# Performance work log

Hardware: AMD Instinct MI355X
Metric: run time of the kernel (lower is better)

Reference implementation:

```python
import jax, jax.numpy as jnp
import numpy as np

B, S, D, H, MEM, P = 32, 512, 768, 8, 768, 3
DK = D // H
LN_EPS = 1e-6


def _layer_norm(x, a, b):
    # torch LayerNorm in source uses unbiased std (ddof=1) and adds eps to std
    mean = x.mean(-1, keepdims=True)
    var = ((x - mean) ** 2).sum(-1, keepdims=True) / (x.shape[-1] - 1)
    return a * (x - mean) / (jnp.sqrt(var) + LN_EPS) + b


def _gcn_branch(x, mask, Wq, bq, Wk, bk, Ws, bs):
    # x: [B,S,D], mask: [B,S] 0/1 ints
    q = (x @ Wq.T + bq).reshape(B, S, H, DK).transpose(0, 2, 1, 3)  # [B,H,S,DK]
    k = (x @ Wk.T + bk).reshape(B, S, H, DK).transpose(0, 2, 1, 3)
    scores = jnp.einsum('bhqd,bhkd->bhqk', q, k) / jnp.sqrt(jnp.float32(DK))
    scores = jnp.where(mask[:, None, None, :] == 0, jnp.float32(-1e9), scores)
    adj = jax.nn.softmax(scores, axis=-1).mean(1)  # average heads -> [B,S,S]
    # adj - diag(diag(adj)) + I  ==  set diagonal to 1
    idx = jnp.arange(S)
    adj = adj.at[:, idx, idx].set(1.0)
    adj = adj * mask[:, :, None].astype(adj.dtype)  # src_mask.transpose(1,2) * adj
    denom = adj.sum(-1, keepdims=True) + 1.0
    out = x
    for W, b in zip(Ws, bs):
        out = jax.nn.relu((adj @ out @ W.T + b) / denom)
    return out, adj


def _proj(a, b):
    # Proj(a, b): (a.b / |b|) * normalize(b)
    b_mo = jnp.sqrt((b * b).sum(-1))
    axb = (a * b).sum(-1)
    bn = b / jnp.maximum(jnp.sqrt((b * b).sum(-1, keepdims=True)), 1e-12)
    return (axb / b_mo)[:, None] * bn


def setup_inputs() -> dict:
    key = jax.random.key(0)
    ks = jax.random.split(key, 32)

    def w(k, shape):
        return jax.random.normal(k, shape, jnp.float32) * 0.02

    inp = {
        'sequence_output': jax.random.normal(ks[0], (B, S, D), jnp.float32),
        'pooled_output': jax.random.normal(ks[1], (B, D), jnp.float32),
        'src_mask': jnp.ones((B, S), jnp.int32),
        'aspect_mask': jnp.ones((B, S), jnp.float32),
        'ln_a': jnp.ones((D,), jnp.float32),
        'ln_b': jnp.zeros((D,), jnp.float32),
        'fp_Wq': w(ks[2], (D, D)), 'fp_bq': jnp.zeros((D,), jnp.float32),
        'fp_Wk': w(ks[3], (D, D)), 'fp_bk': jnp.zeros((D,), jnp.float32),
        'fp_W0': w(ks[4], (MEM, D)), 'fp_b0': jnp.zeros((MEM,), jnp.float32),
        'fp_W1': w(ks[5], (MEM, MEM)), 'fp_b1': jnp.zeros((MEM,), jnp.float32),
        'fc_Wq': w(ks[6], (D, D)), 'fc_bq': jnp.zeros((D,), jnp.float32),
        'fc_Wk': w(ks[7], (D, D)), 'fc_bk': jnp.zeros((D,), jnp.float32),
        'fc_W0': w(ks[8], (MEM, D)), 'fc_b0': jnp.zeros((MEM,), jnp.float32),
        'fc_W1': w(ks[9], (MEM, MEM)), 'fc_b1': jnp.zeros((MEM,), jnp.float32),
        'fp_dense_W': w(ks[10], (P, MEM)), 'fp_dense_b': jnp.zeros((P,), jnp.float32),
        'fc_dense_W': w(ks[11], (P, MEM)), 'fc_dense_b': jnp.zeros((P,), jnp.float32),
    }
    return inp


def reference(sequence_output, pooled_output, src_mask, aspect_mask,
              ln_a, ln_b,
              fp_Wq, fp_bq, fp_Wk, fp_bk, fp_W0, fp_b0, fp_W1, fp_b1,
              fc_Wq, fc_bq, fc_Wk, fc_bk, fc_W0, fc_b0, fc_W1, fc_b1,
              fp_dense_W, fp_dense_b, fc_dense_W, fc_dense_b):
    label_embedding = pooled_output
    att_inputs = _layer_norm(sequence_output, ln_a, ln_b)  # dropout disabled (eval)
    asp_wn = aspect_mask.sum(1)[:, None]  # [B,1]

    fp_out, _ = _gcn_branch(att_inputs, src_mask, fp_Wq, fp_bq, fp_Wk, fp_bk,
                            [fp_W0, fp_W1], [fp_b0, fp_b1])
    fc_out, _ = _gcn_branch(att_inputs, src_mask, fc_Wq, fc_bq, fc_Wk, fc_bk,
                            [fc_W0, fc_W1], [fc_b0, fc_b1])

    outputs_fp = fp_out.sum(1)  # [B,MEM]
    outputs_fc = (fc_out * aspect_mask[:, :, None]).sum(1) / asp_wn  # [B,MEM]

    fp_x = _proj(outputs_fp, outputs_fc)
    fp_y = _proj(outputs_fp, outputs_fp - fp_x)
    fc_y = outputs_fc  # gradient-reverse layer is identity in forward

    logits_p = fp_y @ fp_dense_W.T + fp_dense_b
    logits_c = fc_y @ fc_dense_W.T + fc_dense_b
    return (logits_p, logits_c, fp_y, label_embedding)
```

## Files before the change

kernel.cpp:

```cpp
#include <hip/hip_runtime.h>
#include <math.h>
#include <stdint.h>

#define Bn 32
#define Sn 512
#define Dn 768
#define Hn 8
#define DKn 96
#define Pn 3

typedef __bf16 bf16_t;
typedef bf16_t bf16x8 __attribute__((ext_vector_type(8)));
typedef float f32x4 __attribute__((ext_vector_type(4)));

__device__ __forceinline__ bf16_t f2bf(float f) { return (bf16_t)f; }

__device__ __forceinline__ void gload16(const void* g, void* l) {
    __builtin_amdgcn_global_load_lds((const __attribute__((address_space(1))) void*)g,
                                     (__attribute__((address_space(3))) void*)l, 16, 0, 0);
}

__device__ __forceinline__ float brsum(float v, float* red) {
    int t = threadIdx.x;
    red[t] = v; __syncthreads();
    #pragma unroll
    for (int o = 128; o > 0; o >>= 1) {
        if (t < o) red[t] += red[t + o];
        __syncthreads();
    }
    float r = red[0]; __syncthreads();
    return r;
}

__global__ __launch_bounds__(256) void ln_kernel(const float* __restrict__ in,
                                                 const float* __restrict__ ga,
                                                 const float* __restrict__ gb,
                                                 bf16_t* __restrict__ out) {
    __shared__ float red[256];
    long row = blockIdx.x;
    const float* x = in + row * Dn;
    bf16_t* y = out + row * Dn;
    int t = threadIdx.x;
    float v0 = x[t], v1 = x[t + 256], v2 = x[t + 512];
    float mean = brsum(v0 + v1 + v2, red) / (float)Dn;
    float d0 = v0 - mean, d1 = v1 - mean, d2 = v2 - mean;
    float ss = brsum(d0 * d0 + d1 * d1 + d2 * d2, red);
    float inv = 1.0f / (sqrtf(ss / (float)(Dn - 1)) + 1e-6f);
    y[t]       = f2bf(ga[t]       * d0 * inv + gb[t]);
    y[t + 256] = f2bf(ga[t + 256] * d1 * inv + gb[t + 256]);
    y[t + 512] = f2bf(ga[t + 512] * d2 * inv + gb[t + 512]);
}

__global__ __launch_bounds__(256) void cvt8(const float* __restrict__ s0,
                                            const float* __restrict__ s1,
                                            const float* __restrict__ s2,
                                            const float* __restrict__ s3,
                                            const float* __restrict__ s4,
                                            const float* __restrict__ s5,
                                            const float* __restrict__ s6,
                                            const float* __restrict__ s7,
                                            bf16_t* __restrict__ dst) {
    int y = blockIdx.y;
    const float* s = (y == 0) ? s0 : (y == 1) ? s1 : (y == 2) ? s2 : (y == 3) ? s3
                   : (y == 4) ? s4 : (y == 5) ? s5 : (y == 6) ? s6 : s7;
    long i = (long)blockIdx.x * 1024 + threadIdx.x * 4;
    float4 v = *reinterpret_cast<const float4*>(s + i);
    bf16_t* d = dst + (long)y * Dn * Dn + i;
    d[0] = f2bf(v.x); d[1] = f2bf(v.y); d[2] = f2bf(v.z); d[3] = f2bf(v.w);
}

__global__ __launch_bounds__(256) void biascat_k(const float* __restrict__ s0,
                                                 const float* __restrict__ s1,
                                                 const float* __restrict__ s2,
                                                 const float* __restrict__ s3,
                                                 const float* __restrict__ s4,
                                                 const float* __restrict__ s5,
                                                 const float* __restrict__ s6,
                                                 const float* __restrict__ s7,
                                                 float* __restrict__ dst) {
    int y = blockIdx.x;
    const float* s = (y == 0) ? s0 : (y == 1) ? s1 : (y == 2) ? s2 : (y == 3) ? s3
                   : (y == 4) ? s4 : (y == 5) ? s5 : (y == 6) ? s6 : s7;
    for (int i = threadIdx.x; i < Dn; i += 256) dst[(long)y * Dn + i] = s[i];
}

__global__ void zero_kernel(float* p, int n) {
    int i = blockIdx.x * 256 + threadIdx.x;
    if (i < n) p[i] = 0.0f;
}

template <int EPI>
__global__ __launch_bounds__(256) void gemm_bt(
    const bf16_t* __restrict__ Ag, const bf16_t* __restrict__ Bg,
    bf16_t* __restrict__ Cg, float* __restrict__ outv,
    int lda, int ldb, int ldc, int K,
    long sAhi, long sAlo, long sBhi, long sBlo, long sChi, long sClo,
    int lgZ, float alpha,
    const float* __restrict__ bias, long bias_zs,
    const float* __restrict__ denom,
    const float* __restrict__ aspw) {
    __shared__ __align__(16) bf16_t As[128 * 32];
    __shared__ __align__(16) bf16_t Bs[128 * 32];

    unsigned gx = gridDim.x, gy = gridDim.y;
    unsigned nwg = gx * gy * gridDim.z;
    unsigned flat = (blockIdx.z * gy + blockIdx.y) * gx + blockIdx.x;
    unsigned q8 = nwg >> 3, r8 = nwg & 7;
    unsigned xcd = flat & 7, idx = flat >> 3;
    unsigned swz = (xcd < r8 ? xcd * (q8 + 1) : r8 * (q8 + 1) + (xcd - r8) * q8) + idx;
    unsigned bx = swz % gx;
    unsigned rest = swz / gx;
    unsigned by = rest % gy;
    unsigned zz = rest / gy;
    int zb = zz >> lgZ;
    int zg = zz & ((1 << lgZ) - 1);
    long zful = ((long)zb << lgZ) + zg;

    const bf16_t* A = Ag + zb * sAhi + zg * sAlo;
    const bf16_t* B = Bg + zb * sBhi + zg * sBlo;

    int n0 = bx * 128;
    int m0 = by * 128;
    int tid = threadIdx.x;
    int lane = tid & 63, wv = tid >> 6;
    int wm = wv >> 1, wn = wv & 1;

    int sub = lane >> 2;
    int kcol = (lane & 3) * 8;
    const bf16_t* pA0 = A + (size_t)(m0 + wv * 16 + sub) * lda + kcol;
    const bf16_t* pA1 = pA0 + (size_t)64 * lda;
    const bf16_t* pB0 = B + (size_t)(n0 + wv * 16 + sub) * ldb + kcol;
    const bf16_t* pB1 = pB0 + (size_t)64 * ldb;
    bf16_t* lA0 = As + wv * 512 + lane * 8;
    bf16_t* lA1 = As + (4 + wv) * 512 + lane * 8;
    bf16_t* lB0 = Bs + wv * 512 + lane * 8;
    bf16_t* lB1 = Bs + (4 + wv) * 512 + lane * 8;

    f32x4 acc[4][4];
    #pragma unroll
    for (int i = 0; i < 4; i++)
        #pragma unroll
        for (int j = 0; j < 4; j++) acc[i][j] = (f32x4){0.f, 0.f, 0.f, 0.f};

    const bf16_t* ar = As + (wm * 64 + (lane & 15)) * 32 + (lane >> 4) * 8;
    const bf16_t* br = Bs + (wn * 64 + (lane & 15)) * 32 + (lane >> 4) * 8;

    for (int k0 = 0; k0 < K; k0 += 32) {
        gload16(pA0 + k0, lA0);
        gload16(pA1 + k0, lA1);
        gload16(pB0 + k0, lB0);
        gload16(pB1 + k0, lB1);
        __syncthreads();
        bf16x8 a[4], b[4];
        #pragma unroll
        for (int i = 0; i < 4; i++) a[i] = *(const bf16x8*)(ar + i * 16 * 32);
        #pragma unroll
        for (int j = 0; j < 4; j++) b[j] = *(const bf16x8*)(br + j * 16 * 32);
        #pragma unroll
        for (int i = 0; i < 4; i++)
            #pragma unroll
            for (int j = 0; j < 4; j++)
                acc[i][j] = __builtin_amdgcn_mfma_f32_16x16x32_bf16(a[i], b[j], acc[i][j], 0, 0, 0);
        __syncthreads();
    }

    int nb = n0 + wn * 64 + (lane & 15);
    int mbase = m0 + wm * 64 + (lane >> 4) * 4;
    const float* bz = bias ? bias + zb * bias_zs : nullptr;

    if (EPI == 0) {
        bf16_t* Cz = Cg + zb * sChi + zg * sClo;
        #pragma unroll
        for (int i = 0; i < 4; i++) {
            #pragma unroll
            for (int r = 0; r < 4; r++) {
                long m = mbase + i * 16 + r;
                bf16_t* crow = Cz + m * (long)ldc;
                #pragma unroll
                for (int j = 0; j < 4; j++) {
                    int col = nb + j * 16;
                    float v = acc[i][j][r] * alpha;
                    if (bz) v += bz[col];
                    crow[col] = f2bf(v);
                }
            }
        }
    } else if (EPI == 1) {
        bf16_t* Cz = Cg + zb * sChi + zg * sClo;
        const float* dz = denom + zful * Sn;
        #pragma unroll
        for (int i = 0; i < 4; i++) {
            #pragma unroll
            for (int r = 0; r < 4; r++) {
                int m = mbase + i * 16 + r;
                float dinv = 1.0f / dz[m];
                bf16_t* crow = Cz + (long)m * ldc;
                #pragma unroll
                for (int j = 0; j < 4; j++) {
                    float v = fmaxf((acc[i][j][r] + bz[nb + j * 16]) * dinv, 0.0f);
                    crow[nb + j * 16] = f2bf(v);
                }
            }
        }
    } else {
        const float* dz = denom + zful * Sn;
        float csum[4] = {0.f, 0.f, 0.f, 0.f};
        #pragma unroll
        for (int i = 0; i < 4; i++) {
            #pragma unroll
            for (int r = 0; r < 4; r++) {
                int m = mbase + i * 16 + r;
                float dinv = 1.0f / dz[m];
                float wgt = (aspw && zb) ? aspw[(long)zg * Sn + m] : 1.0f;
                #pragma unroll
                for (int j = 0; j < 4; j++) {
                    float v = fmaxf((acc[i][j][r] + bz[nb + j * 16]) * dinv, 0.0f);
                    csum[j] += v * wgt;
                }
            }
        }
        #pragma unroll
        for (int j = 0; j < 4; j++) {
            float s = csum[j];
            s += __shfl_xor(s, 16);
            s += __shfl_xor(s, 32);
            if (lane < 16) atomicAdd(&outv[zful * Dn + nb + j * 16], s);
        }
    }
}

__global__ __launch_bounds__(256) void fused_adj(
    const bf16_t* __restrict__ QK, bf16_t* __restrict__ adjb,
    float* __restrict__ denomv, const int* __restrict__ mask) {
    __shared__ __align__(16) bf16_t Ks[2][128 * 104];
    __shared__ float red[4][16];

    int L = blockIdx.x;
    int swzi = (L & 7) * 128 + (L >> 3);
    int brc = swzi >> 9;
    int rem = swzi & 511;
    int b = rem >> 4;
    int q0 = (rem & 15) * 32;

    int tid = threadIdx.x;
    int lane = tid & 63, w = tid >> 6;
    int mt = w >> 1, nh = w & 1;
    int g = lane >> 4, c = lane & 15;

    const int LDQ = 3072;
    const bf16_t* Qrow  = QK + ((long)b * Sn + q0 + mt * 16 + c) * LDQ + brc * 1536;
    const bf16_t* Kbase = QK + (long)b * Sn * LDQ + brc * 1536 + Dn;

    const int* mrow = mask + (long)b * Sn;
    unsigned mbits = 0;
    #pragma unroll
    for (int t = 0; t < 4; ++t)
        #pragma unroll
        for (int nj = 0; nj < 4; ++nj)
            if (mrow[t * 128 + nh * 64 + nj * 16 + c] != 0) mbits |= 1u << (t * 4 + nj);

    int srow[6], scc[6];
    #pragma unroll
    for (int p = 0; p < 6; ++p) { int gr = tid + p * 256; srow[p] = gr / 12; scc[p] = gr % 12; }

    f32x4 adjacc[4][4];
    #pragma unroll
    for (int t = 0; t < 4; ++t)
        #pragma unroll
        for (int nj = 0; nj < 4; ++nj) adjacc[t][nj] = (f32x4){0.f, 0.f, 0.f, 0.f};

    f32x4 S[4][4];
    bf16x8 kr0[6], kr1[6], aq[3], aqn[3];
    const float sal = 0.102062072615966f;

    #pragma unroll
    for (int p = 0; p < 6; ++p)
        kr0[p] = *(const bf16x8*)(Kbase + (long)srow[p] * LDQ + scc[p] * 8);
    #pragma unroll
    for (int ks = 0; ks < 3; ++ks)
        aq[ks] = *(const bf16x8*)(Qrow + ks * 32 + g * 8);
    #pragma unroll
    for (int p = 0; p < 6; ++p)
        *(bf16x8*)(&Ks[0][srow[p] * 104 + scc[p] * 8]) = kr0[p];
    #pragma unroll
    for (int p = 0; p < 6; ++p)
        kr1[p] = *(const bf16x8*)(Kbase + (long)(128 + srow[p]) * LDQ + scc[p] * 8);
    __syncthreads();

    for (int h = 0; h < Hn; ++h) {
        #pragma unroll
        for (int t = 0; t < 4; ++t)
            #pragma unroll
            for (int nj = 0; nj < 4; ++nj) S[t][nj] = (f32x4){0.f, 0.f, 0.f, 0.f};

        float rs[4];
        #pragma unroll
        for (int t = 0; t < 4; ++t) {
            int it = h * 4 + t;
            if (it + 2 < 32) {
                int nt = it + 2;
                const bf16_t* kp = Kbase + (long)((nt & 3) * 128) * LDQ + (nt >> 2) * 96;
                if ((t & 1) == 0) {
                    #pragma unroll
                    for (int p = 0; p < 6; ++p)
                        kr0[p] = *(const bf16x8*)(kp + (long)srow[p] * LDQ + scc[p] * 8);
                } else {
                    #pragma unroll
                    for (int p = 0; p < 6; ++p)
                        kr1[p] = *(const bf16x8*)(kp + (long)srow[p] * LDQ + scc[p] * 8);
                }
            }
            if (t == 2 && h < 7) {
                #pragma unroll
                for (int ks = 0; ks < 3; ++ks)
                    aqn[ks] = *(const bf16x8*)(Qrow + (h + 1) * 96 + ks * 32 + g * 8);
            }
            #pragma unroll
            for (int nj = 0; nj < 4; ++nj) {
                #pragma unroll
                for (int ks = 0; ks < 3; ++ks) {
                    bf16x8 bk = *(const bf16x8*)(&Ks[t & 1][(nh * 64 + nj * 16 + c) * 104 + ks * 32 + g * 8]);
                    S[t][nj] = __builtin_amdgcn_mfma_f32_16x16x32_bf16(aq[ks], bk, S[t][nj], 0, 0, 0);
                }
            }
            if (t == 3) {
                rs[0] = rs[1] = rs[2] = rs[3] = 0.f;
                #pragma unroll
                for (int tt = 0; tt < 4; ++tt)
                    #pragma unroll
                    for (int nj = 0; nj < 4; ++nj) {
                        float mkf = ((mbits >> (tt * 4 + nj)) & 1u) ? 1.0f : 0.0f;
                        #pragma unroll
                        for (int ri = 0; ri < 4; ++ri) {
                            float e = mkf * __expf(S[tt][nj][ri] * sal);
                            S[tt][nj][ri] = e;
                            rs[ri] += e;
                        }
                    }
                #pragma unroll
                for (int ri = 0; ri < 4; ++ri) {
                    rs[ri] += __shfl_xor(rs[ri], 1);
                    rs[ri] += __shfl_xor(rs[ri], 2);
                    rs[ri] += __shfl_xor(rs[ri], 4);
                    rs[ri] += __shfl_xor(rs[ri], 8);
                }
                if (c == 0) {
                    #pragma unroll
                    for (int ri = 0; ri < 4; ++ri) red[w][g * 4 + ri] = rs[ri];
                }
            }
            if (it + 1 < 32) {
                if ((t & 1) == 0) {
                    #pragma unroll
                    for (int p = 0; p < 6; ++p)
                        *(bf16x8*)(&Ks[1][srow[p] * 104 + scc[p] * 8]) = kr1[p];
                } else {
                    #pragma unroll
                    for (int p = 0; p < 6; ++p)
                        *(bf16x8*)(&Ks[0][srow[p] * 104 + scc[p] * 8]) = kr0[p];
                }
            }
            __syncthreads();
            if (t == 3) {
                float inv[4];
                #pragma unroll
                for (int ri = 0; ri < 4; ++ri)
                    inv[ri] = 0.125f / (red[w][g * 4 + ri] + red[w ^ 1][g * 4 + ri]);
                #pragma unroll
                for (int tt = 0; tt < 4; ++tt)
                    #pragma unroll
                    for (int nj = 0; nj < 4; ++nj)
                        #pragma unroll
                        for (int ri = 0; ri < 4; ++ri)
                            adjacc[tt][nj][ri] += S[tt][nj][ri] * inv[ri];
                if (h < 7) {
                    #pragma unroll
                    for (int ks = 0; ks < 3; ++ks) aq[ks] = aqn[ks];
                }
            }
        }
    }

    float rm[4];
    #pragma unroll
    for (int ri = 0; ri < 4; ++ri)
        rm[ri] = (mrow[q0 + mt * 16 + g * 4 + ri] != 0) ? 1.0f : 0.0f;
    float rs2[4] = {0.f, 0.f, 0.f, 0.f};
    #pragma unroll
    for (int t = 0; t < 4; ++t)
        #pragma unroll
        for (int nj = 0; nj < 4; ++nj) {
            int n = t * 128 + nh * 64 + nj * 16 + c;
            #pragma unroll
            for (int ri = 0; ri < 4; ++ri) {
                float v = adjacc[t][nj][ri];
                int q = q0 + mt * 16 + g * 4 + ri;
                if (n == q) v = 1.0f;
                v *= rm[ri];
                adjacc[t][nj][ri] = v;
                rs2[ri] += v;
            }
        }
    #pragma unroll
    for (int ri = 0; ri < 4; ++ri) {
        rs2[ri] += __shfl_xor(rs2[ri], 1);
        rs2[ri] += __shfl_xor(rs2[ri], 2);
        rs2[ri] += __shfl_xor(rs2[ri], 4);
        rs2[ri] += __shfl_xor(rs2[ri], 8);
    }
    __syncthreads();
    if (c == 0) {
        #pragma unroll
        for (int ri = 0; ri < 4; ++ri) red[w][g * 4 + ri] = rs2[ri];
    }
    __syncthreads();
    long zful = (long)brc * Bn + b;
    if (nh == 0 && c == 0) {
        #pragma unroll
        for (int ri = 0; ri < 4; ++ri)
            denomv[zful * Sn + q0 + mt * 16 + g * 4 + ri] =
                red[w][g * 4 + ri] + red[w ^ 1][g * 4 + ri] + 1.0f;
    }
    bf16_t* stg = &Ks[0][0];
    #pragma unroll
    for (int t = 0; t < 4; ++t)
        #pragma unroll
        for (int nj = 0; nj < 4; ++nj) {
            int n = t * 128 + nh * 64 + nj * 16 + c;
            #pragma unroll
            for (int ri = 0; ri < 4; ++ri)
                stg[(mt * 16 + g * 4 + ri) * 520 + n] = f2bf(adjacc[t][nj][ri]);
        }
    __syncthreads();
    bf16_t* arow = adjb + (zful * Sn + q0) * Sn;
    #pragma unroll
    for (int p = 0; p < 8; ++p) {
        int gr = tid + p * 256;
        int row = gr >> 6, cc = gr & 63;
        *(bf16x8*)(arow + (long)row * Sn + cc * 8) = *(const bf16x8*)(stg + row * 520 + cc * 8);
    }
}

__global__ __launch_bounds__(256) void final_kernel(const float* __restrict__ ofp,
                                                    const float* __restrict__ ofc_raw,
                                                    const float* __restrict__ aspect,
                                                    const float* __restrict__ pooled,
                                                    const float* __restrict__ fpdW,
                                                    const float* __restrict__ fpdb,
                                                    const float* __restrict__ fcdW,
                                                    const float* __restrict__ fcdb,
                                                    float* __restrict__ out) {
    __shared__ float red[256];
    __shared__ float fp[Dn], fc[Dn], fy[Dn];
    int b = blockIdx.x, t = threadIdx.x;
    float awv = aspect[(long)b * Sn + t] + aspect[(long)b * Sn + t + 256];
    float asp_wn = brsum(awv, red);
    for (int i = t; i < Dn; i += 256) {
        fp[i] = ofp[(long)b * Dn + i];
        fc[i] = ofc_raw[(long)b * Dn + i] / asp_wn;
    }
    __syncthreads();
    float p0 = 0.0f, p1 = 0.0f;
    for (int i = t; i < Dn; i += 256) { p0 += fc[i] * fc[i]; p1 += fp[i] * fc[i]; }
    float dfc2 = brsum(p0, red);
    float dfpfc = brsum(p1, red);
    float bmo = sqrtf(dfc2);
    float coef = dfpfc / bmo;
    float bden = fmaxf(bmo, 1e-12f);
    float q0 = 0.0f, q1 = 0.0f;
    for (int i = t; i < Dn; i += 256) {
        float tv = fp[i] - coef * fc[i] / bden;
        fy[i] = tv;
        q0 += tv * tv;
        q1 += fp[i] * tv;
    }
    float dt2 = brsum(q0, red);
    float dfpt = brsum(q1, red);
    float tmo = sqrtf(dt2);
    float coef2 = dfpt / tmo;
    float tden = fmaxf(tmo, 1e-12f);
    for (int i = t; i < Dn; i += 256) fy[i] = coef2 * fy[i] / tden;
    __syncthreads();
    for (int i = t; i < Dn; i += 256) out[2 * Bn * Pn + (long)b * Dn + i] = fy[i];
    for (int i = t; i < Dn; i += 256)
        out[2 * Bn * Pn + Bn * Dn + (long)b * Dn + i] = pooled[(long)b * Dn + i];
    for (int j = 0; j < Pn; j++) {
        float lp = 0.0f, lc = 0.0f;
        for (int i = t; i < Dn; i += 256) {
            lp += fy[i] * fpdW[(long)j * Dn + i];
            lc += fc[i] * fcdW[(long)j * Dn + i];
        }
        float rp = brsum(lp, red);
        float rc = brsum(lc, red);
        if (t == 0) {
            out[(long)b * Pn + j] = rp + fpdb[j];
            out[Bn * Pn + (long)b * Pn + j] = rc + fcdb[j];
        }
    }
}

extern "C" void kernel_launch(void* const* d_in, const int* in_sizes, int n_in,
                              void* d_out, int out_size, void* d_ws, size_t ws_size,
                              hipStream_t stream) {
    const float* seq     = (const float*)d_in[0];
    const float* pooled  = (const float*)d_in[1];
    const int*   src_msk = (const int*)d_in[2];
    const float* aspect  = (const float*)d_in[3];
    const float* ln_a    = (const float*)d_in[4];
    const float* ln_b    = (const float*)d_in[5];
    float* out = (float*)d_out;

    const long NTD = (long)Bn * Sn * Dn;
    const long NSS = (long)Bn * Sn * Sn;
    const long DD  = (long)Dn * Dn;
    const long SD  = (long)Sn * Dn;

    char* w = (char*)d_ws;
    bf16_t* xbf   = (bf16_t*)w;
    bf16_t* QK    = xbf + NTD;
    bf16_t* H1    = QK;
    bf16_t* XT    = QK + 2 * NTD;
    bf16_t* adjb  = QK + 4 * NTD;
    float*  denom = (float*)(adjb + 2 * NSS);
    float*  ofp   = denom + 2L * Bn * Sn;
    float*  bcat  = ofp + 2L * Bn * Dn;
    bf16_t* Wb    = (bf16_t*)(bcat + 8 * Dn);

    ln_kernel<<<dim3(Bn * Sn), dim3(256), 0, stream>>>(seq, ln_a, ln_b, xbf);
    zero_kernel<<<dim3((2 * Bn * Dn + 255) / 256), dim3(256), 0, stream>>>(ofp, 2 * Bn * Dn);

    cvt8<<<dim3(576, 8), dim3(256), 0, stream>>>(
        (const float*)d_in[6], (const float*)d_in[8],
        (const float*)d_in[14], (const float*)d_in[16],
        (const float*)d_in[10], (const float*)d_in[18],
        (const float*)d_in[12], (const float*)d_in[20], Wb);
    biascat_k<<<dim3(8), dim3(256), 0, stream>>>(
        (const float*)d_in[7], (const float*)d_in[9],
        (const float*)d_in[15], (const float*)d_in[17],
        (const float*)d_in[11], (const float*)d_in[19],
        (const float*)d_in[13], (const float*)d_in[21], bcat);

    gemm_bt<0><<<dim3(24, 128, 1), dim3(256), 0, stream>>>(
        xbf, Wb, QK, nullptr, Dn, Dn, 3072, Dn,
        0, 0, 0, 0, 0, 0, 0, 1.0f, bcat, 0, nullptr, nullptr);

    fused_adj<<<dim3(2 * Bn * Sn / 32), dim3(256), 0, stream>>>(QK, adjb, denom, src_msk);

    gemm_bt<0><<<dim3(4, 6, 64), dim3(256), 0, stream>>>(
        Wb + 4 * DD, xbf, XT, nullptr, Dn, Dn, Sn, Dn,
        DD, 0, 0, SD, 32 * SD, SD,
        5, 1.0f, nullptr, 0, nullptr, nullptr);

    gemm_bt<1><<<dim3(6, 4, 64), dim3(256), 0, stream>>>(
        adjb, XT, H1, nullptr, Sn, Sn, Dn, Sn,
        32L * Sn * Sn, (long)Sn * Sn, 32 * SD, SD, 32 * SD, SD,
        5, 1.0f, bcat + 4 * Dn, Dn, denom, nullptr);

    gemm_bt<0><<<dim3(4, 6, 64), dim3(256), 0, stream>>>(
        Wb + 6 * DD, H1, XT, nullptr, Dn, Dn, Sn, Dn,
        DD, 0, 32 * SD, SD, 32 * SD, SD,
        5, 1.0f, nullptr, 0, nullptr, nullptr);

    gemm_bt<2><<<dim3(6, 4, 64), dim3(256), 0, stream>>>(
        adjb, XT, nullptr, ofp, Sn, Sn, 0, Sn,
        32L * Sn * Sn, (long)Sn * Sn, 32 * SD, SD, 0, 0,
        5, 1.0f, bcat + 6 * Dn, Dn, denom, aspect);

    final_kernel<<<dim3(Bn), dim3(256), 0, stream>>>(
        ofp, ofp + (long)Bn * Dn, aspect, pooled,
        (const float*)d_in[22], (const float*)d_in[23],
        (const float*)d_in[24], (const float*)d_in[25], out);
}
```

Before: 516.6 us.

## Replace 128x128 GEMM with 256x256 tile, 4-stage LDS pipeline, 8 waves

Replaces the single-buffered 128x128 GEMM with a 512-thread 256x256 tile kernel. It uses a 4-deep ring of LDS buffers with three tiles prefetched ahead, explicit vmcnt waits, split half-tile MFMA phases and setprio around the MFMA blocks. The aim is to hide global-load latency, which the old version exposed with two syncthreads per K step, and to raise arithmetic intensity per workgroup. The cost is fewer workgroups (as few as 384 for the batched GEMMs), which lowers occupancy and risks load imbalance across CUs. The 128KB of LDS also limits each CU to one block.

```diff
diff --git a/kernel.cpp b/kernel.cpp
--- a/kernel.cpp
+++ b/kernel.cpp
@@ -90,17 +90,16 @@
 }
 
 template <int EPI>
-__global__ __launch_bounds__(256) void gemm_bt(
+__global__ __launch_bounds__(512, 1) void gemm256(
     const bf16_t* __restrict__ Ag, const bf16_t* __restrict__ Bg,
     bf16_t* __restrict__ Cg, float* __restrict__ outv,
     int lda, int ldb, int ldc, int K,
     long sAhi, long sAlo, long sBhi, long sBlo, long sChi, long sClo,
-    int lgZ, float alpha,
+    int lgZ,
     const float* __restrict__ bias, long bias_zs,
     const float* __restrict__ denom,
     const float* __restrict__ aspw) {
-    __shared__ __align__(16) bf16_t As[128 * 32];
-    __shared__ __align__(16) bf16_t Bs[128 * 32];
+    __shared__ __align__(16) bf16_t lds[4][2][8192];
 
     unsigned gx = gridDim.x, gy = gridDim.y;
     unsigned nwg = gx * gy * gridDim.z;
@@ -114,72 +113,116 @@
     unsigned zz = rest / gy;
     int zb = zz >> lgZ;
     int zg = zz & ((1 << lgZ) - 1);
-    long zful = ((long)zb << lgZ) + zg;
+    long zful = zz;
 
     const bf16_t* A = Ag + zb * sAhi + zg * sAlo;
     const bf16_t* B = Bg + zb * sBhi + zg * sBlo;
 
-    int n0 = bx * 128;
-    int m0 = by * 128;
+    int n0 = bx * 256, m0 = by * 256;
     int tid = threadIdx.x;
-    int lane = tid & 63, wv = tid >> 6;
-    int wm = wv >> 1, wn = wv & 1;
-
-    int sub = lane >> 2;
-    int kcol = (lane & 3) * 8;
-    const bf16_t* pA0 = A + (size_t)(m0 + wv * 16 + sub) * lda + kcol;
-    const bf16_t* pA1 = pA0 + (size_t)64 * lda;
-    const bf16_t* pB0 = B + (size_t)(n0 + wv * 16 + sub) * ldb + kcol;
-    const bf16_t* pB1 = pB0 + (size_t)64 * ldb;
-    bf16_t* lA0 = As + wv * 512 + lane * 8;
-    bf16_t* lA1 = As + (4 + wv) * 512 + lane * 8;
-    bf16_t* lB0 = Bs + wv * 512 + lane * 8;
-    bf16_t* lB1 = Bs + (4 + wv) * 512 + lane * 8;
-
-    f32x4 acc[4][4];
-    #pragma unroll
-    for (int i = 0; i < 4; i++)
-        #pragma unroll
-        for (int j = 0; j < 4; j++) acc[i][j] = (f32x4){0.f, 0.f, 0.f, 0.f};
-
-    const bf16_t* ar = As + (wm * 64 + (lane & 15)) * 32 + (lane >> 4) * 8;
-    const bf16_t* br = Bs + (wn * 64 + (lane & 15)) * 32 + (lane >> 4) * 8;
-
-    for (int k0 = 0; k0 < K; k0 += 32) {
-        gload16(pA0 + k0, lA0);
-        gload16(pA1 + k0, lA1);
-        gload16(pB0 + k0, lB0);
-        gload16(pB1 + k0, lB1);
-        __syncthreads();
+    int lane = tid & 63, w = tid >> 6;
+    int wm = w >> 2, wn = w & 3;
+
+    const int NT = K >> 5;
+
+    int srow = lane & 15;
+    int skc = (lane >> 4) * 8;
+    const bf16_t* Asrc0 = A + (size_t)(m0 + (w * 2 + 0) * 16 + srow) * lda + skc;
+    const bf16_t* Asrc1 = A + (size_t)(m0 + (w * 2 + 1) * 16 + srow) * lda + skc;
+    const bf16_t* Bsrc0 = B + (size_t)(n0 + (w * 2 + 0) * 16 + srow) * ldb + skc;
+    const bf16_t* Bsrc1 = B + (size_t)(n0 + (w * 2 + 1) * 16 + srow) * ldb + skc;
+    int c0off = (w * 2 + 0) * 512 + lane * 8;
+    int c1off = (w * 2 + 1) * 512 + lane * 8;
+
+    f32x4 acc[8][4];
+    #pragma unroll
+    for (int i = 0; i < 8; ++i)
+        #pragma unroll
+        for (int j = 0; j < 4; ++j) acc[i][j] = (f32x4){0.f, 0.f, 0.f, 0.f};
+
+    #pragma unroll
+    for (int tt = 0; tt < 3; ++tt) {
+        gload16(Asrc0 + tt * 32, &lds[tt][0][c0off]);
+        gload16(Asrc1 + tt * 32, &lds[tt][0][c1off]);
+        gload16(Bsrc0 + tt * 32, &lds[tt][1][c0off]);
+        gload16(Bsrc1 + tt * 32, &lds[tt][1][c1off]);
+    }
+    asm volatile("s_waitcnt vmcnt(8)" ::: "memory");
+    __builtin_amdgcn_s_barrier();
+
+    int aoff = wm * 8 * 512 + lane * 8;
+    int boff = wn * 4 * 512 + lane * 8;
+
+    for (int t = 0; t < NT; ++t) {
+        const bf16_t* bufA = &lds[t & 3][0][0];
+        const bf16_t* bufB = &lds[t & 3][1][0];
+        int tn = t + 3;
+        bf16_t* dA = &lds[tn & 3][0][0];
+        bf16_t* dB = &lds[tn & 3][1][0];
+        bool st = tn < NT;
+
         bf16x8 a[4], b[4];
         #pragma unroll
-        for (int i = 0; i < 4; i++) a[i] = *(const bf16x8*)(ar + i * 16 * 32);
-        #pragma unroll
-        for (int j = 0; j < 4; j++) b[j] = *(const bf16x8*)(br + j * 16 * 32);
-        #pragma unroll
-        for (int i = 0; i < 4; i++)
-            #pragma unroll
-            for (int j = 0; j < 4; j++)
+        for (int i = 0; i < 4; ++i)
+            a[i] = *(const bf16x8*)(bufA + aoff + i * 512);
+        #pragma unroll
+        for (int j = 0; j < 4; ++j)
+            b[j] = *(const bf16x8*)(bufB + boff + j * 512);
+        if (st) {
+            gload16(Asrc0 + tn * 32, dA + c0off);
+            gload16(Bsrc0 + tn * 32, dB + c0off);
+        }
+        __builtin_amdgcn_s_barrier();
+        asm volatile("s_waitcnt lgkmcnt(0)" ::: "memory");
+        __builtin_amdgcn_sched_barrier(0);
+        __builtin_amdgcn_s_setprio(1);
+        #pragma unroll
+        for (int i = 0; i < 4; ++i)
+            #pragma unroll
+            for (int j = 0; j < 4; ++j)
                 acc[i][j] = __builtin_amdgcn_mfma_f32_16x16x32_bf16(a[i], b[j], acc[i][j], 0, 0, 0);
-        __syncthreads();
+        __builtin_amdgcn_s_setprio(0);
+        __builtin_amdgcn_s_barrier();
+
+        #pragma unroll
+        for (int i = 0; i < 4; ++i)
+            a[i] = *(const bf16x8*)(bufA + aoff + (4 + i) * 512);
+        if (st) {
+            gload16(Asrc1 + tn * 32, dA + c1off);
+            gload16(Bsrc1 + tn * 32, dB + c1off);
+        }
+        __builtin_amdgcn_s_barrier();
+        asm volatile("s_waitcnt lgkmcnt(0)" ::: "memory");
+        __builtin_amdgcn_sched_barrier(0);
+        __builtin_amdgcn_s_setprio(1);
+        #pragma unroll
+        for (int i = 0; i < 4; ++i)
+            #pragma unroll
+            for (int j = 0; j < 4; ++j)
+                acc[4 + i][j] = __builtin_amdgcn_mfma_f32_16x16x32_bf16(a[i], b[j], acc[4 + i][j], 0, 0, 0);
+        __builtin_amdgcn_s_setprio(0);
+        if (t + 3 < NT)      asm volatile("s_waitcnt vmcnt(8)" ::: "memory");
+        else if (t + 2 < NT) asm volatile("s_waitcnt vmcnt(4)" ::: "memory");
+        else                 asm volatile("s_waitcnt vmcnt(0)" ::: "memory");
+        __builtin_amdgcn_s_barrier();
     }
 
     int nb = n0 + wn * 64 + (lane & 15);
-    int mbase = m0 + wm * 64 + (lane >> 4) * 4;
+    int mbase = m0 + wm * 128 + (lane >> 4) * 4;
     const float* bz = bias ? bias + zb * bias_zs : nullptr;
 
     if (EPI == 0) {
         bf16_t* Cz = Cg + zb * sChi + zg * sClo;
         #pragma unroll
-        for (int i = 0; i < 4; i++) {
-            #pragma unroll
-            for (int r = 0; r < 4; r++) {
+        for (int i = 0; i < 8; ++i) {
+            #pragma unroll
+            for (int r = 0; r < 4; ++r) {
                 long m = mbase + i * 16 + r;
                 bf16_t* crow = Cz + m * (long)ldc;
                 #pragma unroll
-                for (int j = 0; j < 4; j++) {
+                for (int j = 0; j < 4; ++j) {
                     int col = nb + j * 16;
-                    float v = acc[i][j][r] * alpha;
+                    float v = acc[i][j][r];
                     if (bz) v += bz[col];
                     crow[col] = f2bf(v);
                 }
@@ -189,14 +232,14 @@
         bf16_t* Cz = Cg + zb * sChi + zg * sClo;
         const float* dz = denom + zful * Sn;
         #pragma unroll
-        for (int i = 0; i < 4; i++) {
-            #pragma unroll
-            for (int r = 0; r < 4; r++) {
+        for (int i = 0; i < 8; ++i) {
+            #pragma unroll
+            for (int r = 0; r < 4; ++r) {
                 int m = mbase + i * 16 + r;
                 float dinv = 1.0f / dz[m];
                 bf16_t* crow = Cz + (long)m * ldc;
                 #pragma unroll
-                for (int j = 0; j < 4; j++) {
+                for (int j = 0; j < 4; ++j) {
                     float v = fmaxf((acc[i][j][r] + bz[nb + j * 16]) * dinv, 0.0f);
                     crow[nb + j * 16] = f2bf(v);
                 }
@@ -206,21 +249,21 @@
         const float* dz = denom + zful * Sn;
         float csum[4] = {0.f, 0.f, 0.f, 0.f};
         #pragma unroll
-        for (int i = 0; i < 4; i++) {
-            #pragma unroll
-            for (int r = 0; r < 4; r++) {
+        for (int i = 0; i < 8; ++i) {
+            #pragma unroll
+            for (int r = 0; r < 4; ++r) {
                 int m = mbase + i * 16 + r;
                 float dinv = 1.0f / dz[m];
                 float wgt = (aspw && zb) ? aspw[(long)zg * Sn + m] : 1.0f;
                 #pragma unroll
-                for (int j = 0; j < 4; j++) {
+                for (int j = 0; j < 4; ++j) {
                     float v = fmaxf((acc[i][j][r] + bz[nb + j * 16]) * dinv, 0.0f);
                     csum[j] += v * wgt;
                 }
             }
         }
         #pragma unroll
-        for (int j = 0; j < 4; j++) {
+        for (int j = 0; j < 4; ++j) {
             float s = csum[j];
             s += __shfl_xor(s, 16);
             s += __shfl_xor(s, 32);
@@ -540,31 +583,31 @@
         (const float*)d_in[11], (const float*)d_in[19],
         (const float*)d_in[13], (const float*)d_in[21], bcat);
 
-    gemm_bt<0><<<dim3(24, 128, 1), dim3(256), 0, stream>>>(
+    gemm256<0><<<dim3(12, 64, 1), dim3(512), 0, stream>>>(
         xbf, Wb, QK, nullptr, Dn, Dn, 3072, Dn,
-        0, 0, 0, 0, 0, 0, 0, 1.0f, bcat, 0, nullptr, nullptr);
+        0, 0, 0, 0, 0, 0, 0, bcat, 0, nullptr, nullptr);
 
     fused_adj<<<dim3(2 * Bn * Sn / 32), dim3(256), 0, stream>>>(QK, adjb, denom, src_msk);
 
-    gemm_bt<0><<<dim3(4, 6, 64), dim3(256), 0, stream>>>(
+    gemm256<0><<<dim3(2, 3, 64), dim3(512), 0, stream>>>(
         Wb + 4 * DD, xbf, XT, nullptr, Dn, Dn, Sn, Dn,
         DD, 0, 0, SD, 32 * SD, SD,
-        5, 1.0f, nullptr, 0, nullptr, nullptr);
-
-    gemm_bt<1><<<dim3(6, 4, 64), dim3(256), 0, stream>>>(
+        5, nullptr, 0, nullptr, nullptr);
+
+    gemm256<1><<<dim3(3, 2, 64), dim3(512), 0, stream>>>(
         adjb, XT, H1, nullptr, Sn, Sn, Dn, Sn,
         32L * Sn * Sn, (long)Sn * Sn, 32 * SD, SD, 32 * SD, SD,
-        5, 1.0f, bcat + 4 * Dn, Dn, denom, nullptr);
-
-    gemm_bt<0><<<dim3(4, 6, 64), dim3(256), 0, stream>>>(
+        5, bcat + 4 * Dn, Dn, denom, nullptr);
+
+    gemm256<0><<<dim3(2, 3, 64), dim3(512), 0, stream>>>(
         Wb + 6 * DD, H1, XT, nullptr, Dn, Dn, Sn, Dn,
         DD, 0, 32 * SD, SD, 32 * SD, SD,
-        5, 1.0f, nullptr, 0, nullptr, nullptr);
-
-    gemm_bt<2><<<dim3(6, 4, 64), dim3(256), 0, stream>>>(
+        5, nullptr, 0, nullptr, nullptr);
+
+    gemm256<2><<<dim3(3, 2, 64), dim3(512), 0, stream>>>(
         adjb, XT, nullptr, ofp, Sn, Sn, 0, Sn,
         32L * Sn * Sn, (long)Sn * Sn, 32 * SD, SD, 0, 0,
-        5, 1.0f, bcat + 6 * Dn, Dn, denom, aspect);
+        5, bcat + 6 * Dn, Dn, denom, aspect);
 
     final_kernel<<<dim3(Bn), dim3(256), 0, stream>>>(
         ofp, ofp + (long)Bn * Dn, aspect, pooled,
```

Measured after the change: 513.9 us. Within noise of the previous version (-0.5%).
